# Performance work log

Measured on AMD Instinct MI355X. Metric: run time of the kernel, lower is better.

## Reference

```python
import jax, jax.numpy as jnp
import numpy as np

N = 50000        # nodes
E = 800000       # edges (avg degree 16)
F_NODE = 128     # node feature dim
F_EDGE = 8       # edge feature dim
H_ATT = 64       # attention hidden dim
H = 8            # attention heads
P = 16           # propagation dim per head (H*P = 128)


def setup_inputs() -> dict:
    key = jax.random.key(0)
    ks = jax.random.split(key, 16)
    s = lambda fan_in: 1.0 / np.sqrt(fan_in)
    return {
        "feat": jax.random.normal(ks[0], (N, F_NODE), jnp.float32),
        "feat_edge": jax.random.normal(ks[1], (E, F_EDGE), jnp.float32),
        "src": jax.random.randint(ks[2], (E,), 0, N, jnp.int32),
        "dst": jax.random.randint(ks[3], (E,), 0, N, jnp.int32),
        # attention MLPs (no bias), stored as [in, out]
        "w_att_src0": jax.random.normal(ks[4], (F_NODE, H_ATT), jnp.float32) * s(F_NODE),
        "w_att_src1": jax.random.normal(ks[5], (H_ATT, H), jnp.float32) * s(H_ATT),
        "w_att_dst0": jax.random.normal(ks[6], (F_NODE, H_ATT), jnp.float32) * s(F_NODE),
        "w_att_dst1": jax.random.normal(ks[7], (H_ATT, H), jnp.float32) * s(H_ATT),
        "w_att_edge0": jax.random.normal(ks[8], (F_EDGE, H_ATT), jnp.float32) * s(F_EDGE),
        "w_att_edge1": jax.random.normal(ks[9], (H_ATT, H), jnp.float32) * s(H_ATT),
        # propagation projections (single layer: Linear(F_NODE, H*P) with bias)
        "w_prop_src": jax.random.normal(ks[10], (F_NODE, H * P), jnp.float32) * s(F_NODE),
        "b_prop_src": jnp.zeros((H * P,), jnp.float32),
        "w_prop_dst": jax.random.normal(ks[11], (F_NODE, H * P), jnp.float32) * s(F_NODE),
        "b_prop_dst": jnp.zeros((H * P,), jnp.float32),
    }


def reference(feat, feat_edge, src, dst,
              w_att_src0, w_att_src1, w_att_dst0, w_att_dst1,
              w_att_edge0, w_att_edge1,
              w_prop_src, b_prop_src, w_prop_dst, b_prop_dst):
    relu = jax.nn.relu
    n = feat.shape[0]

    # propagation branch: [N, H*P] -> [N, H, P]
    prop_src = (feat @ w_prop_src + b_prop_src).reshape(n, H, P)
    prop_dst = (feat @ w_prop_dst + b_prop_dst).reshape(n, H, P)

    # attention MLPs -> per-node / per-edge head logits [*, H]
    a_src = relu(feat @ w_att_src0) @ w_att_src1          # [N, H]
    a_dst = relu(feat @ w_att_dst0) @ w_att_dst1          # [N, H]
    a_edge = relu(feat_edge @ w_att_edge0) @ w_att_edge1  # [E, H]

    # per-edge attention logit: relu(a_src[u] + a_dst[v] + a_edge)
    att = relu(a_src[src] + a_dst[dst] + a_edge)          # [E, H]

    # edge softmax over incoming edges of each destination node (per head)
    m = jax.ops.segment_max(att, dst, num_segments=n)     # [N, H]
    ex = jnp.exp(att - m[dst])                            # [E, H]
    denom = jax.ops.segment_sum(ex, dst, num_segments=n)  # [N, H]
    alpha = ex / jnp.maximum(denom[dst], 1e-16)           # [E, H]

    # message = prop_src[u] * alpha, sum-aggregate to destinations
    msg = prop_src[src] * alpha[:, :, None]               # [E, H, P]
    agg = jax.ops.segment_sum(msg, dst, num_segments=n)   # [N, H, P]

    # n_hiddens_agg == []: residual add of prop_dst
    return agg + prop_dst
```

## Files before the change

kernel.cpp:

```cpp
#include <hip/hip_runtime.h>
#include <hip/hip_bf16.h>

#define NODECAP 48
#define NPB 256
#define BCAP 4608
#define MAXBUCK 256
#define PART_CHUNK 1600
#define EPART_BLOCKS 500
#define SLICES 8

typedef __attribute__((ext_vector_type(8))) short bf16x8;
typedef __attribute__((ext_vector_type(4))) float f32x4;

static __device__ __forceinline__ short f2b(float f) {
    __hip_bfloat16 h = __float2bfloat16(f);
    return *reinterpret_cast<short*>(&h);
}
static __device__ __forceinline__ float b2f(unsigned short u) {
    union { unsigned int i; float f; } v; v.i = ((unsigned int)u) << 16; return v.f;
}

__global__ __launch_bounds__(256) void pack_w(
    const float* __restrict__ w_ps, const float* __restrict__ w_pd,
    const float* __restrict__ w_as0, const float* __restrict__ w_ad0,
    short* __restrict__ wp, short* __restrict__ wa, int* __restrict__ gcnt, int nbuck)
{
    const int idx = blockIdx.x * 256 + threadIdx.x;
    if (idx < 256 * 128) {
        const int c = idx >> 7, k = idx & 127;
        const float v = (c < 128) ? w_ps[(size_t)k * 128 + c] : w_pd[(size_t)k * 128 + (c - 128)];
        wp[idx] = f2b(v);
    } else if (idx < 256 * 128 + 128 * 128) {
        const int j = idx - 256 * 128;
        const int c = j >> 7, k = j & 127;
        const float v = (c < 64) ? w_as0[(size_t)k * 64 + c] : w_ad0[(size_t)k * 64 + (c - 64)];
        wa[j] = f2b(v);
    }
    if (idx < nbuck) gcnt[idx] = 0;
}

__global__ __launch_bounds__(256) void node_mfma(
    const float* __restrict__ feat,
    const short* __restrict__ wp, const short* __restrict__ wa,
    const float* __restrict__ b_ps, const float* __restrict__ b_pd,
    const float* __restrict__ w_as1, const float* __restrict__ w_ad1,
    signed char* __restrict__ prop_i8, float* __restrict__ scale_g,
    short* __restrict__ pd_bf,
    short* __restrict__ a_src_bf, float* __restrict__ a_dst, int n)
{
    __shared__ unsigned char afb[32 * 256];
    __shared__ short ht[32][137];
    __shared__ int rowmax_i[32];
    const int t = threadIdx.x;
    const int lane = t & 63;
    const int wid = t >> 6;
    const int l15 = lane & 15;
    const int l4 = lane >> 4;
    const int base = blockIdx.x * 32;

    if (t < 32) rowmax_i[t] = 0;

    #pragma unroll
    for (int i = 0; i < 2; ++i) {
        const int chunk = t + i * 256;
        const int row = chunk >> 4;
        const int kc = chunk & 15;
        const int grow = base + row;
        float f[8];
        if (grow < n) {
            const float4 v0 = *reinterpret_cast<const float4*>(feat + (size_t)grow * 128 + kc * 8);
            const float4 v1 = *reinterpret_cast<const float4*>(feat + (size_t)grow * 128 + kc * 8 + 4);
            f[0] = v0.x; f[1] = v0.y; f[2] = v0.z; f[3] = v0.w;
            f[4] = v1.x; f[5] = v1.y; f[6] = v1.z; f[7] = v1.w;
        } else {
            #pragma unroll
            for (int j = 0; j < 8; ++j) f[j] = 0.f;
        }
        short h8[8];
        #pragma unroll
        for (int j = 0; j < 8; ++j) h8[j] = f2b(f[j]);
        const int byte = (row * 256 + kc * 16) ^ ((row & 7) << 4);
        *reinterpret_cast<bf16x8*>(afb + byte) = *reinterpret_cast<const bf16x8*>(h8);
    }
    __syncthreads();

    {
        f32x4 acc[2][4] = {};
        for (int kk = 0; kk < 4; ++kk) {
            bf16x8 a[2], b[4];
            #pragma unroll
            for (int rt = 0; rt < 2; ++rt) {
                const int arow = rt * 16 + l15;
                const int ab = (arow * 256 + kk * 64 + l4 * 16) ^ ((arow & 7) << 4);
                a[rt] = *reinterpret_cast<const bf16x8*>(afb + ab);
            }
            #pragma unroll
            for (int c = 0; c < 4; ++c) {
                const int col = (wid * 4 + c) * 16 + l15;
                b[c] = *reinterpret_cast<const bf16x8*>(wp + (size_t)col * 128 + kk * 32 + l4 * 8);
            }
            #pragma unroll
            for (int rt = 0; rt < 2; ++rt)
                #pragma unroll
                for (int c = 0; c < 4; ++c)
                    acc[rt][c] = __builtin_amdgcn_mfma_f32_16x16x32_bf16(a[rt], b[c], acc[rt][c], 0, 0, 0);
        }

        if (wid < 2) {
            #pragma unroll
            for (int rt = 0; rt < 2; ++rt)
                #pragma unroll
                for (int r = 0; r < 4; ++r) {
                    float m = 0.f;
                    #pragma unroll
                    for (int c = 0; c < 4; ++c) {
                        const int col = (wid * 4 + c) * 16 + l15;
                        m = fmaxf(m, fabsf(acc[rt][c][r] + b_ps[col]));
                    }
                    atomicMax(&rowmax_i[rt * 16 + l4 * 4 + r], __float_as_int(m));
                }
        }
        __syncthreads();

        #pragma unroll
        for (int c = 0; c < 4; ++c) {
            const int col = (wid * 4 + c) * 16 + l15;
            const bool sr = (col < 128);
            const float bias = sr ? b_ps[col] : b_pd[col - 128];
            #pragma unroll
            for (int rt = 0; rt < 2; ++rt)
                #pragma unroll
                for (int r = 0; r < 4; ++r) {
                    const int rl = rt * 16 + l4 * 4 + r;
                    const int row = base + rl;
                    if (row < n) {
                        const float v = acc[rt][c][r] + bias;
                        if (sr) {
                            const float rm = __int_as_float(rowmax_i[rl]);
                            const float inv = 127.f / fmaxf(rm, 1e-20f);
                            prop_i8[(size_t)row * 128 + col] = (signed char)lrintf(v * inv);
                        } else {
                            pd_bf[(size_t)row * 128 + (col - 128)] = f2b(v);
                        }
                    }
                }
        }
        if (t < 32) {
            const int row = base + t;
            if (row < n)
                scale_g[row] = fmaxf(__int_as_float(rowmax_i[t]), 1e-20f) / 127.f;
        }
    }

    {
        f32x4 acc[2][2] = {};
        for (int kk = 0; kk < 4; ++kk) {
            bf16x8 a[2], b[2];
            #pragma unroll
            for (int rt = 0; rt < 2; ++rt) {
                const int arow = rt * 16 + l15;
                const int ab = (arow * 256 + kk * 64 + l4 * 16) ^ ((arow & 7) << 4);
                a[rt] = *reinterpret_cast<const bf16x8*>(afb + ab);
            }
            #pragma unroll
            for (int c = 0; c < 2; ++c) {
                const int col = (wid * 2 + c) * 16 + l15;
                b[c] = *reinterpret_cast<const bf16x8*>(wa + (size_t)col * 128 + kk * 32 + l4 * 8);
            }
            #pragma unroll
            for (int rt = 0; rt < 2; ++rt)
                #pragma unroll
                for (int c = 0; c < 2; ++c)
                    acc[rt][c] = __builtin_amdgcn_mfma_f32_16x16x32_bf16(a[rt], b[c], acc[rt][c], 0, 0, 0);
        }
        #pragma unroll
        for (int c = 0; c < 2; ++c) {
            const int col = (wid * 2 + c) * 16 + l15;
            #pragma unroll
            for (int rt = 0; rt < 2; ++rt)
                #pragma unroll
                for (int r = 0; r < 4; ++r)
                    ht[rt * 16 + l4 * 4 + r][col] = f2b(fmaxf(acc[rt][c][r], 0.f));
        }
    }
    __syncthreads();

    #pragma unroll
    for (int o = 0; o < 2; ++o) {
        const int idx = t + o * 256;
        const int i = idx >> 4;
        const int hh = idx & 15;
        const bool is_src = (hh < 8);
        const int h = is_src ? hh : (hh - 8);
        const float* w1 = is_src ? w_as1 : w_ad1;
        const int jb = is_src ? 0 : 64;
        float acc = 0.f;
        #pragma unroll
        for (int j = 0; j < 64; ++j)
            acc += b2f((unsigned short)ht[i][jb + j]) * w1[j * 8 + h];
        const int row = base + i;
        if (row < n) {
            if (is_src) a_src_bf[(size_t)row * 8 + h] = f2b(acc);
            else        a_dst[(size_t)row * 8 + h] = acc;
        }
    }
}

__global__ __launch_bounds__(256) void edge_part(
    const int* __restrict__ src, const int* __restrict__ dst,
    const float* __restrict__ feat_edge,
    const float* __restrict__ w_e0, const float* __restrict__ w_e1,
    const short* __restrict__ a_src_bf,
    int* __restrict__ gcnt, int2* __restrict__ part, short* __restrict__ ax,
    int E, int nbuck)
{
    __shared__ int hist[MAXBUCK];
    __shared__ int cursor[MAXBUCK];
    __shared__ int dcache[PART_CHUNK];
    const int t = threadIdx.x;

    if (blockIdx.x < EPART_BLOCKS) {
        const int e0 = blockIdx.x * PART_CHUNK;
        const int e1 = min(e0 + PART_CHUNK, E);

        for (int i = t; i < nbuck; i += 256) hist[i] = 0;
        __syncthreads();
        for (int e = e0 + t; e < e1; e += 256) {
            const int d = dst[e];
            dcache[e - e0] = d;
            atomicAdd(&hist[d >> 8], 1);
        }
        __syncthreads();
        for (int i = t; i < nbuck; i += 256) {
            const int c = hist[i];
            cursor[i] = (c > 0) ? atomicAdd(&gcnt[i], c) : 0;
        }
        __syncthreads();
        for (int e = e0 + t; e < e1; e += 256) {
            const int d = dcache[e - e0];
            const int s = src[e];
            const int b = d >> 8;
            const int pos = atomicAdd(&cursor[b], 1);
            if (pos < BCAP)
                part[(size_t)b * BCAP + pos] = make_int2((e << 8) | (d & 255), s);
        }
        return;
    }

    const int e = (blockIdx.x - EPART_BLOCKS) * 256 + t;
    if (e >= E) return;

    float fe[8];
    const float4 v0 = *reinterpret_cast<const float4*>(feat_edge + (size_t)e * 8);
    const float4 v1 = *reinterpret_cast<const float4*>(feat_edge + (size_t)e * 8 + 4);
    fe[0] = v0.x; fe[1] = v0.y; fe[2] = v0.z; fe[3] = v0.w;
    fe[4] = v1.x; fe[5] = v1.y; fe[6] = v1.z; fe[7] = v1.w;

    float ae[8] = {};
    #pragma unroll 8
    for (int j = 0; j < 64; ++j) {
        float hj = 0.f;
        #pragma unroll
        for (int k = 0; k < 8; ++k) hj += fe[k] * w_e0[k * 64 + j];
        hj = fmaxf(hj, 0.f);
        #pragma unroll
        for (int hh = 0; hh < 8; ++hh) ae[hh] += hj * w_e1[j * 8 + hh];
    }

    const int s = src[e];
    const ushort4 as0 = *reinterpret_cast<const ushort4*>(a_src_bf + (size_t)s * 8);
    const ushort4 as1 = *reinterpret_cast<const ushort4*>(a_src_bf + (size_t)s * 8 + 4);
    short eb[8];
    eb[0] = f2b(ae[0] + b2f(as0.x)); eb[1] = f2b(ae[1] + b2f(as0.y));
    eb[2] = f2b(ae[2] + b2f(as0.z)); eb[3] = f2b(ae[3] + b2f(as0.w));
    eb[4] = f2b(ae[4] + b2f(as1.x)); eb[5] = f2b(ae[5] + b2f(as1.y));
    eb[6] = f2b(ae[6] + b2f(as1.z)); eb[7] = f2b(ae[7] + b2f(as1.w));
    *reinterpret_cast<uint4*>(ax + (size_t)e * 8) = *reinterpret_cast<const uint4*>(eb);
}

__global__ __launch_bounds__(256) void bucket_agg(
    const int2* __restrict__ part, const int* __restrict__ gcnt,
    const short* __restrict__ ax, const float* __restrict__ a_dst,
    const signed char* __restrict__ prop_i8, const float* __restrict__ scale_g,
    const short* __restrict__ pd_bf,
    float* __restrict__ out, int n)
{
    __shared__ int2  lists[32][NODECAP];
    __shared__ int   lcnt[32];
    __shared__ float adst_s[32][8];
    const int t = threadIdx.x;
    const int b = blockIdx.x >> 3;
    const int slice = blockIdx.x & 7;
    const int node0 = (b << 8) + (slice << 5);

    if (t < 32) lcnt[t] = 0;
    {
        const int r = t >> 3, h = t & 7;
        const int nd = node0 + r;
        adst_s[r][h] = (nd < n) ? a_dst[(size_t)nd * 8 + h] : 0.f;
    }
    __syncthreads();

    const int cnt = min(gcnt[b], BCAP);
    const int2* pb = part + (size_t)b * BCAP;
    for (int j = t; j < cnt; j += 256) {
        const int2 pr = pb[j];
        const int dlow = pr.x & 255;
        if ((dlow >> 5) == slice) {
            const int r = dlow & 31;
            const int slot = atomicAdd(&lcnt[r], 1);
            if (slot < NODECAP) lists[r][slot] = make_int2(pr.x >> 8, pr.y);
        }
    }
    __syncthreads();

    const int grp = t >> 4;
    const int l = t & 15;
    const int h = l >> 1;
    const int half = l & 1;
    const int eoff = h * 16 + half * 8;

    union I2C { int2 i; signed char c[8]; };

    for (int r = grp; r < 32; r += 16) {
        const int node = node0 + r;
        if (node >= n) continue;
        int deg = lcnt[r];
        if (deg > NODECAP) deg = NODECAP;
        const float adv = adst_s[r][h];

        const ushort4 pda = *reinterpret_cast<const ushort4*>(
            pd_bf + (size_t)node * 128 + eoff);
        const ushort4 pdb = *reinterpret_cast<const ushort4*>(
            pd_bf + (size_t)node * 128 + eoff + 4);

        float dsumv = 0.f;
        float acc[8] = {};
        for (int j0 = 0; j0 < deg; j0 += 8) {
            float at[8]; float sc[8]; I2C pv[8];
            #pragma unroll
            for (int u = 0; u < 8; ++u) {
                const int j = j0 + u;
                const bool act = (j < deg);
                const int2 pr = lists[r][act ? j : 0];
                at[u] = b2f((unsigned short)ax[(size_t)pr.x * 8 + h]);
                sc[u] = scale_g[pr.y];
                pv[u].i = *reinterpret_cast<const int2*>(
                    prop_i8 + (size_t)pr.y * 128 + eoff);
            }
            #pragma unroll
            for (int u = 0; u < 8; ++u) {
                const bool act = (j0 + u < deg);
                const float ex = act ? __expf(fmaxf(at[u] + adv, 0.f)) : 0.f;
                dsumv += ex;
                const float exsc = ex * sc[u];
                #pragma unroll
                for (int k = 0; k < 8; ++k)
                    acc[k] += exsc * (float)pv[u].c[k];
            }
        }
        const float dinv = 1.f / fmaxf(dsumv, 1e-16f);

        f32x4 o0, o1;
        o0[0] = b2f(pda.x) + acc[0] * dinv; o0[1] = b2f(pda.y) + acc[1] * dinv;
        o0[2] = b2f(pda.z) + acc[2] * dinv; o0[3] = b2f(pda.w) + acc[3] * dinv;
        o1[0] = b2f(pdb.x) + acc[4] * dinv; o1[1] = b2f(pdb.y) + acc[5] * dinv;
        o1[2] = b2f(pdb.z) + acc[6] * dinv; o1[3] = b2f(pdb.w) + acc[7] * dinv;
        float* op = out + (size_t)node * 128 + eoff;
        __builtin_nontemporal_store(o0, reinterpret_cast<f32x4*>(op));
        __builtin_nontemporal_store(o1, reinterpret_cast<f32x4*>(op + 4));
    }
}

extern "C" void kernel_launch(void* const* d_in, const int* in_sizes, int n_in,
                              void* d_out, int out_size, void* d_ws, size_t ws_size,
                              hipStream_t stream)
{
    const float* feat      = (const float*)d_in[0];
    const float* feat_edge = (const float*)d_in[1];
    const int*   src       = (const int*)d_in[2];
    const int*   dst       = (const int*)d_in[3];
    const float* w_as0     = (const float*)d_in[4];
    const float* w_as1     = (const float*)d_in[5];
    const float* w_ad0     = (const float*)d_in[6];
    const float* w_ad1     = (const float*)d_in[7];
    const float* w_e0      = (const float*)d_in[8];
    const float* w_e1      = (const float*)d_in[9];
    const float* w_ps      = (const float*)d_in[10];
    const float* b_ps      = (const float*)d_in[11];
    const float* w_pd      = (const float*)d_in[12];
    const float* b_pd      = (const float*)d_in[13];

    const int n = in_sizes[0] / 128;
    const int E = in_sizes[2];
    const int nbuck = (n + NPB - 1) / NPB;
    float* out = (float*)d_out;

    signed char* prop_i8 = (signed char*)d_ws;
    float* scale_g = (float*)(prop_i8 + (size_t)n * 128);
    short* pd_bf   = (short*)(scale_g + n);
    short* a_src_bf = pd_bf + (size_t)n * 128;
    float* a_dst = (float*)(a_src_bf + (size_t)n * 8);
    int*   gcnt  = (int*)(a_dst + (size_t)n * 8);
    int2*  part  = (int2*)(gcnt + ((nbuck + 1) & ~1));
    short* ax    = (short*)(part + (size_t)nbuck * BCAP);
    short* wp    = ax + (size_t)E * 8;
    short* wa    = wp + 256 * 128;

    pack_w<<<192, 256, 0, stream>>>(
        w_ps, w_pd, w_as0, w_ad0, wp, wa, gcnt, nbuck);

    node_mfma<<<(n + 31) / 32, 256, 0, stream>>>(
        feat, wp, wa, b_ps, b_pd, w_as1, w_ad1,
        prop_i8, scale_g, pd_bf, a_src_bf, a_dst, n);

    const int axBlocks = (E + 255) / 256;
    edge_part<<<EPART_BLOCKS + axBlocks, 256, 0, stream>>>(
        src, dst, feat_edge, w_e0, w_e1, a_src_bf, gcnt, part, ax, E, nbuck);

    bucket_agg<<<nbuck * SLICES, 256, 0, stream>>>(
        part, gcnt, ax, a_dst, prop_i8, scale_g, pd_bf, out, n);
}
```

Baseline: 140.5 us.

## Stage node_mfma outputs in LDS for coalesced stores and use 64-row tiles

```diff
diff --git a/kernel.cpp b/kernel.cpp
--- a/kernel.cpp
+++ b/kernel.cpp
@@ -48,20 +48,24 @@
     short* __restrict__ pd_bf,
     short* __restrict__ a_src_bf, float* __restrict__ a_dst, int n)
 {
-    __shared__ unsigned char afb[32 * 256];
-    __shared__ short ht[32][137];
-    __shared__ int rowmax_i[32];
+    __shared__ __align__(16) char smraw[42112];
+    __shared__ int rowmax_i[64];
+    unsigned char* afb = (unsigned char*)smraw;
+    short* ht = (short*)(smraw + 16384);
+    short* pdtile = (short*)smraw;
+    signed char* qtile = (signed char*)(smraw + 33920);
+
     const int t = threadIdx.x;
     const int lane = t & 63;
     const int wid = t >> 6;
     const int l15 = lane & 15;
     const int l4 = lane >> 4;
-    const int base = blockIdx.x * 32;
-
-    if (t < 32) rowmax_i[t] = 0;
+    const int base = blockIdx.x * 64;
+
+    if (t < 64) rowmax_i[t] = 0;
 
     #pragma unroll
-    for (int i = 0; i < 2; ++i) {
+    for (int i = 0; i < 4; ++i) {
         const int chunk = t + i * 256;
         const int row = chunk >> 4;
         const int kc = chunk & 15;
@@ -84,109 +88,103 @@
     }
     __syncthreads();
 
+    f32x4 acc_p[4][4] = {};
+    for (int kk = 0; kk < 4; ++kk) {
+        bf16x8 a[4], b[4];
+        #pragma unroll
+        for (int rt = 0; rt < 4; ++rt) {
+            const int arow = rt * 16 + l15;
+            const int ab = (arow * 256 + kk * 64 + l4 * 16) ^ ((arow & 7) << 4);
+            a[rt] = *reinterpret_cast<const bf16x8*>(afb + ab);
+        }
+        #pragma unroll
+        for (int c = 0; c < 4; ++c) {
+            const int col = (wid * 4 + c) * 16 + l15;
+            b[c] = *reinterpret_cast<const bf16x8*>(wp + (size_t)col * 128 + kk * 32 + l4 * 8);
+        }
+        #pragma unroll
+        for (int rt = 0; rt < 4; ++rt)
+            #pragma unroll
+            for (int c = 0; c < 4; ++c)
+                acc_p[rt][c] = __builtin_amdgcn_mfma_f32_16x16x32_bf16(a[rt], b[c], acc_p[rt][c], 0, 0, 0);
+    }
+
     {
-        f32x4 acc[2][4] = {};
+        f32x4 acc_h[4][2] = {};
         for (int kk = 0; kk < 4; ++kk) {
-            bf16x8 a[2], b[4];
-            #pragma unroll
-            for (int rt = 0; rt < 2; ++rt) {
+            bf16x8 a[4], b[2];
+            #pragma unroll
+            for (int rt = 0; rt < 4; ++rt) {
                 const int arow = rt * 16 + l15;
                 const int ab = (arow * 256 + kk * 64 + l4 * 16) ^ ((arow & 7) << 4);
                 a[rt] = *reinterpret_cast<const bf16x8*>(afb + ab);
             }
             #pragma unroll
-            for (int c = 0; c < 4; ++c) {
-                const int col = (wid * 4 + c) * 16 + l15;
-                b[c] = *reinterpret_cast<const bf16x8*>(wp + (size_t)col * 128 + kk * 32 + l4 * 8);
-            }
-            #pragma unroll
-            for (int rt = 0; rt < 2; ++rt)
-                #pragma unroll
-                for (int c = 0; c < 4; ++c)
-                    acc[rt][c] = __builtin_amdgcn_mfma_f32_16x16x32_bf16(a[rt], b[c], acc[rt][c], 0, 0, 0);
-        }
-
-        if (wid < 2) {
-            #pragma unroll
-            for (int rt = 0; rt < 2; ++rt)
-                #pragma unroll
-                for (int r = 0; r < 4; ++r) {
-                    float m = 0.f;
-                    #pragma unroll
-                    for (int c = 0; c < 4; ++c) {
-                        const int col = (wid * 4 + c) * 16 + l15;
-                        m = fmaxf(m, fabsf(acc[rt][c][r] + b_ps[col]));
-                    }
-                    atomicMax(&rowmax_i[rt * 16 + l4 * 4 + r], __float_as_int(m));
-                }
-        }
-        __syncthreads();
-
-        #pragma unroll
-        for (int c = 0; c < 4; ++c) {
-            const int col = (wid * 4 + c) * 16 + l15;
-            const bool sr = (col < 128);
-            const float bias = sr ? b_ps[col] : b_pd[col - 128];
-            #pragma unroll
-            for (int rt = 0; rt < 2; ++rt)
-                #pragma unroll
-                for (int r = 0; r < 4; ++r) {
-                    const int rl = rt * 16 + l4 * 4 + r;
-                    const int row = base + rl;
-                    if (row < n) {
-                        const float v = acc[rt][c][r] + bias;
-                        if (sr) {
-                            const float rm = __int_as_float(rowmax_i[rl]);
-                            const float inv = 127.f / fmaxf(rm, 1e-20f);
-                            prop_i8[(size_t)row * 128 + col] = (signed char)lrintf(v * inv);
-                        } else {
-                            pd_bf[(size_t)row * 128 + (col - 128)] = f2b(v);
-                        }
-                    }
-                }
-        }
-        if (t < 32) {
-            const int row = base + t;
-            if (row < n)
-                scale_g[row] = fmaxf(__int_as_float(rowmax_i[t]), 1e-20f) / 127.f;
-        }
-    }
-
-    {
-        f32x4 acc[2][2] = {};
-        for (int kk = 0; kk < 4; ++kk) {
-            bf16x8 a[2], b[2];
-            #pragma unroll
-            for (int rt = 0; rt < 2; ++rt) {
-                const int arow = rt * 16 + l15;
-                const int ab = (arow * 256 + kk * 64 + l4 * 16) ^ ((arow & 7) << 4);
-                a[rt] = *reinterpret_cast<const bf16x8*>(afb + ab);
-            }
-            #pragma unroll
             for (int c = 0; c < 2; ++c) {
                 const int col = (wid * 2 + c) * 16 + l15;
                 b[c] = *reinterpret_cast<const bf16x8*>(wa + (size_t)col * 128 + kk * 32 + l4 * 8);
             }
             #pragma unroll
-            for (int rt = 0; rt < 2; ++rt)
+            for (int rt = 0; rt < 4; ++rt)
                 #pragma unroll
                 for (int c = 0; c < 2; ++c)
-                    acc[rt][c] = __builtin_amdgcn_mfma_f32_16x16x32_bf16(a[rt], b[c], acc[rt][c], 0, 0, 0);
+                    acc_h[rt][c] = __builtin_amdgcn_mfma_f32_16x16x32_bf16(a[rt], b[c], acc_h[rt][c], 0, 0, 0);
         }
         #pragma unroll
         for (int c = 0; c < 2; ++c) {
             const int col = (wid * 2 + c) * 16 + l15;
             #pragma unroll
-            for (int rt = 0; rt < 2; ++rt)
+            for (int rt = 0; rt < 4; ++rt)
                 #pragma unroll
                 for (int r = 0; r < 4; ++r)
-                    ht[rt * 16 + l4 * 4 + r][col] = f2b(fmaxf(acc[rt][c][r], 0.f));
-        }
+                    ht[(rt * 16 + l4 * 4 + r) * 137 + col] = f2b(fmaxf(acc_h[rt][c][r], 0.f));
+        }
+    }
+
+    if (wid < 2) {
+        #pragma unroll
+        for (int rt = 0; rt < 4; ++rt)
+            #pragma unroll
+            for (int r = 0; r < 4; ++r) {
+                float m = 0.f;
+                #pragma unroll
+                for (int c = 0; c < 4; ++c) {
+                    const int col = (wid * 4 + c) * 16 + l15;
+                    m = fmaxf(m, fabsf(acc_p[rt][c][r] + b_ps[col]));
+                }
+                atomicMax(&rowmax_i[rt * 16 + l4 * 4 + r], __float_as_int(m));
+            }
     }
     __syncthreads();
 
     #pragma unroll
-    for (int o = 0; o < 2; ++o) {
+    for (int c = 0; c < 4; ++c) {
+        const int col = (wid * 4 + c) * 16 + l15;
+        const bool sr = (col < 128);
+        const float bias = sr ? b_ps[col] : b_pd[col - 128];
+        #pragma unroll
+        for (int rt = 0; rt < 4; ++rt)
+            #pragma unroll
+            for (int r = 0; r < 4; ++r) {
+                const int rl = rt * 16 + l4 * 4 + r;
+                const float v = acc_p[rt][c][r] + bias;
+                if (sr) {
+                    const float rm = __int_as_float(rowmax_i[rl]);
+                    const float inv = 127.f / fmaxf(rm, 1e-20f);
+                    qtile[rl * 128 + col] = (signed char)lrintf(v * inv);
+                } else {
+                    pdtile[rl * 128 + (col - 128)] = f2b(v);
+                }
+            }
+    }
+    if (t < 64) {
+        const int row = base + t;
+        if (row < n)
+            scale_g[row] = fmaxf(__int_as_float(rowmax_i[t]), 1e-20f) / 127.f;
+    }
+
+    #pragma unroll
+    for (int o = 0; o < 4; ++o) {
         const int idx = t + o * 256;
         const int i = idx >> 4;
         const int hh = idx & 15;
@@ -197,12 +195,32 @@
         float acc = 0.f;
         #pragma unroll
         for (int j = 0; j < 64; ++j)
-            acc += b2f((unsigned short)ht[i][jb + j]) * w1[j * 8 + h];
+            acc += b2f((unsigned short)ht[i * 137 + jb + j]) * w1[j * 8 + h];
         const int row = base + i;
         if (row < n) {
             if (is_src) a_src_bf[(size_t)row * 8 + h] = f2b(acc);
             else        a_dst[(size_t)row * 8 + h] = acc;
         }
+    }
+    __syncthreads();
+
+    #pragma unroll
+    for (int i = 0; i < 2; ++i) {
+        const int idx = t + i * 256;
+        const int row = idx >> 3, seg = idx & 7;
+        const int grow = base + row;
+        if (grow < n)
+            *reinterpret_cast<int4*>(prop_i8 + (size_t)grow * 128 + seg * 16) =
+                *reinterpret_cast<const int4*>(qtile + row * 128 + seg * 16);
+    }
+    #pragma unroll
+    for (int i = 0; i < 4; ++i) {
+        const int idx = t + i * 256;
+        const int row = idx >> 4, seg = idx & 15;
+        const int grow = base + row;
+        if (grow < n)
+            *reinterpret_cast<int4*>(pd_bf + (size_t)grow * 128 + seg * 8) =
+                *reinterpret_cast<const int4*>(pdtile + row * 128 + seg * 8);
     }
 }
 
@@ -410,7 +428,7 @@
     pack_w<<<192, 256, 0, stream>>>(
         w_ps, w_pd, w_as0, w_ad0, wp, wa, gcnt, nbuck);
 
-    node_mfma<<<(n + 31) / 32, 256, 0, stream>>>(
+    node_mfma<<<(n + 63) / 64, 256, 0, stream>>>(
         feat, wp, wa, b_ps, b_pd, w_as1, w_ad1,
         prop_i8, scale_g, pd_bf, a_src_bf, a_dst, n);
 
```

After: 143.2 us. Within noise of the previous version (+2.0%).
